# Kernel tuning notes

Hardware: AMD Instinct MI355X
Metric: run time of the kernel (lower is better)

## Reference

```python
import jax, jax.numpy as jnp
import numpy as np

N = 5_120_000  # x_lim_num * y_lim_num * z_lim_num = 400*400*32 pseudo voxel centers


def setup_inputs() -> dict:
    key = jax.random.key(0)
    k1, k2 = jax.random.split(key)
    # per-point scales (exp(log sqrt knn-dist)) are small positive values
    scales = jax.random.uniform(k1, (N, 3), jnp.float32, 0.05, 0.5)
    # quaternions (build_rotation normalizes them itself)
    rots = jax.random.normal(k2, (N, 4), jnp.float32)
    return {"scales": scales, "rots": rots}


def _build_rotation(q):
    # normalize quaternion, mirror torch build_rotation
    q = q / jnp.sqrt(jnp.sum(q * q, axis=1, keepdims=True))
    r, x, y, z = q[:, 0], q[:, 1], q[:, 2], q[:, 3]
    R = jnp.stack([
        1 - 2 * (y * y + z * z), 2 * (x * y - r * z),     2 * (x * z + r * y),
        2 * (x * y + r * z),     1 - 2 * (x * x + z * z), 2 * (y * z - r * x),
        2 * (x * z - r * y),     2 * (y * z + r * x),     1 - 2 * (x * x + y * y),
    ], axis=-1)
    return R.reshape(-1, 3, 3)  # [N,3,3]


def reference(scales, rots):
    # build_covariance_from_scaling_rotation(scales, scaling_modifier=1, rots)
    R = _build_rotation(rots)                 # [N,3,3]
    L = R * scales[:, None, :]                # R @ diag(s): scale columns of R
    cov = jnp.einsum('nij,nkj->nik', L, L)    # L @ L^T, [N,3,3] symmetric
    # strip_symmetric: upper-triangular 6-vector
    symm = jnp.stack([cov[:, 0, 0], cov[:, 0, 1], cov[:, 0, 2],
                      cov[:, 1, 1], cov[:, 1, 2], cov[:, 2, 2]], axis=1)
    return symm  # [N,6]
```

## Files before the change

kernel.cpp:

```cpp
#include <hip/hip_runtime.h>


typedef float f32x4 __attribute__((ext_vector_type(4)));

__device__ __forceinline__ void cov6(float r, float x, float y, float z,
                                     float s0, float s1, float s2,
                                     float* __restrict__ o) {
    float inv = rsqrtf(r * r + x * x + y * y + z * z);
    r *= inv; x *= inv; y *= inv; z *= inv;
    float R00 = 1.f - 2.f * (y * y + z * z);
    float R01 = 2.f * (x * y - r * z);
    float R02 = 2.f * (x * z + r * y);
    float R10 = 2.f * (x * y + r * z);
    float R11 = 1.f - 2.f * (x * x + z * z);
    float R12 = 2.f * (y * z - r * x);
    float R20 = 2.f * (x * z - r * y);
    float R21 = 2.f * (y * z + r * x);
    float R22 = 1.f - 2.f * (x * x + y * y);
    float a = s0 * s0, b = s1 * s1, c = s2 * s2;
    o[0] = R00 * R00 * a + R01 * R01 * b + R02 * R02 * c;
    o[1] = R00 * R10 * a + R01 * R11 * b + R02 * R12 * c;
    o[2] = R00 * R20 * a + R01 * R21 * b + R02 * R22 * c;
    o[3] = R10 * R10 * a + R11 * R11 * b + R12 * R12 * c;
    o[4] = R10 * R20 * a + R11 * R21 * b + R12 * R22 * c;
    o[5] = R20 * R20 * a + R21 * R21 * b + R22 * R22 * c;
}

__device__ __forceinline__ int swz(int g) { return g ^ ((g >> 3) & 1); }

__global__ __launch_bounds__(128) void gaus_cov_wave(
    const float* __restrict__ scales,
    const float* __restrict__ rots,
    float* __restrict__ out,
    int n) {
    __shared__ f32x4 lds[768];
    const int t = threadIdx.x;
    const int w = t >> 6;
    const int l = t & 63;
    const long long blockRow = 512ll * blockIdx.x;

    if (blockRow + 512 <= n) {
        const long long gt = blockRow / 4 + t;
        const float4* sp = reinterpret_cast<const float4*>(scales + 12ll * gt);
        float4 s0 = sp[0], s1 = sp[1], s2 = sp[2];
        const float4* rp = reinterpret_cast<const float4*>(rots + 16ll * gt);
        float4 q0 = rp[0], q1 = rp[1], q2 = rp[2], q3 = rp[3];
        float o[24];
        cov6(q0.x, q0.y, q0.z, q0.w, s0.x, s0.y, s0.z, o);
        cov6(q1.x, q1.y, q1.z, q1.w, s0.w, s1.x, s1.y, o + 6);
        cov6(q2.x, q2.y, q2.z, q2.w, s1.z, s1.w, s2.x, o + 12);
        cov6(q3.x, q3.y, q3.z, q3.w, s2.y, s2.z, s2.w, o + 18);
        #pragma unroll
        for (int j = 0; j < 6; ++j) {
            f32x4 v = {o[4 * j], o[4 * j + 1], o[4 * j + 2], o[4 * j + 3]};
            lds[swz(6 * t + j)] = v;
        }
        __builtin_amdgcn_wave_barrier();
        asm volatile("s_waitcnt lgkmcnt(0)" ::: "memory");
        __builtin_amdgcn_sched_barrier(0);
        f32x4* op = reinterpret_cast<f32x4*>(out) + 768ll * blockIdx.x;
        #pragma unroll
        for (int k = 0; k < 6; ++k) {
            int g = 384 * w + 64 * k + l;
            f32x4 v = lds[swz(g)];
            __builtin_nontemporal_store(v, op + g);
        }
    } else {
        for (int rr = 0; rr < 4; ++rr) {
            long long r = blockRow + 4ll * t + rr;
            if (r >= n) break;
            float a0 = scales[3ll * r + 0];
            float a1 = scales[3ll * r + 1];
            float a2 = scales[3ll * r + 2];
            const float4* rp = reinterpret_cast<const float4*>(rots + 4ll * r);
            float4 q = rp[0];
            float o[6];
            cov6(q.x, q.y, q.z, q.w, a0, a1, a2, o);
            float* op = out + 6ll * r;
            op[0] = o[0]; op[1] = o[1]; op[2] = o[2];
            op[3] = o[3]; op[4] = o[4]; op[5] = o[5];
        }
    }
}

extern "C" void kernel_launch(void* const* d_in, const int* in_sizes, int n_in,
                              void* d_out, int out_size, void* d_ws, size_t ws_size,
                              hipStream_t stream) {
    const float* scales = (const float*)d_in[0];
    const float* rots   = (const float*)d_in[1];
    float* out = (float*)d_out;
    int n = in_sizes[0] / 3;
    int nblocks = (int)((n + 511ll) / 512ll);
    gaus_cov_wave<<<nblocks, 128, 0, stream>>>(scales, rots, out, n);
}
```

Before: 43.75 us.

## Convert to persistent grid-stride kernel with register prefetch of next tile

Replaces the one-block-per-512-rows launch with a capped persistent grid of up to 2048 blocks. Each block loops over tiles and issues the global loads for its next tile while it computes and stores the current one. The ragged tail is moved into block 0 as a simple strided loop. The aim is to overlap load latency with compute and stores and to cut block launch overhead, at the cost of fewer resident waves per CU and serialized tail work in one block.

```diff
diff --git a/kernel.cpp b/kernel.cpp
--- a/kernel.cpp
+++ b/kernel.cpp
@@ -28,28 +28,59 @@
 
 __device__ __forceinline__ int swz(int g) { return g ^ ((g >> 3) & 1); }
 
-__global__ __launch_bounds__(128) void gaus_cov_wave(
+__global__ __launch_bounds__(128) void gaus_cov_pipe(
     const float* __restrict__ scales,
     const float* __restrict__ rots,
     float* __restrict__ out,
-    int n) {
+    int n, int nfull) {
     __shared__ f32x4 lds[768];
     const int t = threadIdx.x;
     const int w = t >> 6;
     const int l = t & 63;
-    const long long blockRow = 512ll * blockIdx.x;
 
-    if (blockRow + 512 <= n) {
-        const long long gt = blockRow / 4 + t;
+    if (blockIdx.x == 0) {
+        for (long long r = 512ll * nfull + t; r < n; r += 128) {
+            float a0 = scales[3 * r + 0], a1 = scales[3 * r + 1], a2 = scales[3 * r + 2];
+            const float4* rp = reinterpret_cast<const float4*>(rots + 4 * r);
+            float4 q = rp[0];
+            float o[6];
+            cov6(q.x, q.y, q.z, q.w, a0, a1, a2, o);
+            float* op = out + 6 * r;
+            op[0] = o[0]; op[1] = o[1]; op[2] = o[2];
+            op[3] = o[3]; op[4] = o[4]; op[5] = o[5];
+        }
+    }
+
+    int cid = blockIdx.x;
+    if (cid >= nfull) return;
+
+    float4 s0, s1, s2, q0, q1, q2, q3;
+    {
+        const long long gt = 128ll * cid + t;
         const float4* sp = reinterpret_cast<const float4*>(scales + 12ll * gt);
-        float4 s0 = sp[0], s1 = sp[1], s2 = sp[2];
+        s0 = sp[0]; s1 = sp[1]; s2 = sp[2];
         const float4* rp = reinterpret_cast<const float4*>(rots + 16ll * gt);
-        float4 q0 = rp[0], q1 = rp[1], q2 = rp[2], q3 = rp[3];
+        q0 = rp[0]; q1 = rp[1]; q2 = rp[2]; q3 = rp[3];
+    }
+
+    while (true) {
+        const int nxt = cid + (int)gridDim.x;
+        const bool have_next = nxt < nfull;
+
         float o[24];
         cov6(q0.x, q0.y, q0.z, q0.w, s0.x, s0.y, s0.z, o);
         cov6(q1.x, q1.y, q1.z, q1.w, s0.w, s1.x, s1.y, o + 6);
         cov6(q2.x, q2.y, q2.z, q2.w, s1.z, s1.w, s2.x, o + 12);
         cov6(q3.x, q3.y, q3.z, q3.w, s2.y, s2.z, s2.w, o + 18);
+
+        if (have_next) {
+            const long long gt = 128ll * nxt + t;
+            const float4* sp = reinterpret_cast<const float4*>(scales + 12ll * gt);
+            s0 = sp[0]; s1 = sp[1]; s2 = sp[2];
+            const float4* rp = reinterpret_cast<const float4*>(rots + 16ll * gt);
+            q0 = rp[0]; q1 = rp[1]; q2 = rp[2]; q3 = rp[3];
+        }
+
         #pragma unroll
         for (int j = 0; j < 6; ++j) {
             f32x4 v = {o[4 * j], o[4 * j + 1], o[4 * j + 2], o[4 * j + 3]};
@@ -58,28 +89,15 @@
         __builtin_amdgcn_wave_barrier();
         asm volatile("s_waitcnt lgkmcnt(0)" ::: "memory");
         __builtin_amdgcn_sched_barrier(0);
-        f32x4* op = reinterpret_cast<f32x4*>(out) + 768ll * blockIdx.x;
+        f32x4* op = reinterpret_cast<f32x4*>(out) + 768ll * cid;
         #pragma unroll
         for (int k = 0; k < 6; ++k) {
             int g = 384 * w + 64 * k + l;
             f32x4 v = lds[swz(g)];
             __builtin_nontemporal_store(v, op + g);
         }
-    } else {
-        for (int rr = 0; rr < 4; ++rr) {
-            long long r = blockRow + 4ll * t + rr;
-            if (r >= n) break;
-            float a0 = scales[3ll * r + 0];
-            float a1 = scales[3ll * r + 1];
-            float a2 = scales[3ll * r + 2];
-            const float4* rp = reinterpret_cast<const float4*>(rots + 4ll * r);
-            float4 q = rp[0];
-            float o[6];
-            cov6(q.x, q.y, q.z, q.w, a0, a1, a2, o);
-            float* op = out + 6ll * r;
-            op[0] = o[0]; op[1] = o[1]; op[2] = o[2];
-            op[3] = o[3]; op[4] = o[4]; op[5] = o[5];
-        }
+        if (!have_next) break;
+        cid = nxt;
     }
 }
 
@@ -90,6 +108,7 @@
     const float* rots   = (const float*)d_in[1];
     float* out = (float*)d_out;
     int n = in_sizes[0] / 3;
-    int nblocks = (int)((n + 511ll) / 512ll);
-    gaus_cov_wave<<<nblocks, 128, 0, stream>>>(scales, rots, out, n);
+    int nfull = (int)(n / 512ll);
+    int grid = nfull < 2048 ? (nfull > 0 ? nfull : 1) : 2048;
+    gaus_cov_pipe<<<grid, 128, 0, stream>>>(scales, rots, out, n, nfull);
 }
```

After: 44.39 us. No clear change (+1.5%).
